# Optimization experiments

Measured on AMD Instinct MI355X. Metric: run time of the kernel, lower is better.

The kernel has to match this reference:

```python
import jax, jax.numpy as jnp
import numpy as np

B, S, D, H = 4, 2048, 768, 12


def setup_inputs() -> dict:
    key = jax.random.key(0)
    k1, k2, k3, k4 = jax.random.split(key, 4)
    std = D ** (-0.5)
    x = jax.random.normal(k1, (B, S, D), dtype=jnp.float32)
    W_QKV = jax.random.normal(k2, (3, D, D), dtype=jnp.float32) * std
    W_O = jax.random.normal(k3, (D, D), dtype=jnp.float32) * std
    token_positions = jnp.sort(jax.random.randint(k4, (B, S), 0, S), axis=-1).astype(jnp.int64)
    return {"x": x, "W_QKV": W_QKV, "W_O": W_O, "token_positions": token_positions,
            "num_heads": H, "theta": 10000}


def _apply_rope(t, cos, sin):
    # t: (B, H, S, Hd); cos/sin: (B, 1, S, Hd/2). Interleaved even/odd pairs.
    te, to = t[..., 0::2], t[..., 1::2]
    re = te * cos - to * sin
    ro = te * sin + to * cos
    return jnp.stack([re, ro], axis=-1).reshape(t.shape)


def reference(x, W_QKV, W_O, token_positions, num_heads, theta):
    b, s, d = x.shape
    hd = d // num_heads  # d_head = d_k = d_v
    # fused QKV projection: Q = x @ W_QKV[0].T etc.
    qkv = jnp.einsum('bsd,kod->kbso', x, W_QKV)              # (3, B, S, D)
    qkv = qkv.reshape(3, b, s, num_heads, hd).transpose(0, 1, 3, 2, 4)  # (3, B, H, S, Hd)
    q, k, v = qkv[0], qkv[1], qkv[2]
    # RoPE angles: pos * theta^(-2j/d_k)
    inv_freq = jnp.asarray(theta, x.dtype) ** (-(jnp.arange(0, hd, 2, dtype=x.dtype) / hd))
    angles = token_positions.astype(x.dtype)[..., None] * inv_freq    # (B, S, Hd/2)
    cos = jnp.cos(angles)[:, None]                                     # (B, 1, S, Hd/2)
    sin = jnp.sin(angles)[:, None]
    q = _apply_rope(q, cos, sin)
    k = _apply_rope(k, cos, sin)
    # causal attention
    scores = jnp.einsum('bhqd,bhkd->bhqk', q, k) / (hd ** 0.5)        # (B, H, S, S)
    causal = jnp.tril(jnp.ones((s, s), dtype=bool))
    scores = jnp.where(causal, scores, -jnp.inf)
    probs = jax.nn.softmax(scores, axis=-1)
    out = jnp.einsum('bhqk,bhkd->bhqd', probs, v)                      # (B, H, S, Hd)
    out = out.transpose(0, 2, 1, 3).reshape(b, s, d)
    return out @ W_O.T
```

## Files before the change

kernel.cpp:

```cpp
#include <hip/hip_runtime.h>
#include <hip/hip_bf16.h>

typedef __bf16 bf16;
typedef __bf16 bf16x8 __attribute__((ext_vector_type(8)));
typedef __bf16 bf16x4 __attribute__((ext_vector_type(4)));
typedef short  s16x4  __attribute__((ext_vector_type(4)));
typedef float  f32x4  __attribute__((ext_vector_type(4)));

#if defined(__has_builtin)
#if __has_builtin(__builtin_amdgcn_mfma_f32_16x16x16bf16_1k)
#define HAVE_MFMA16 1
#endif
#endif

__device__ __forceinline__ void gl_lds16(const void* g, void* l) {
  __builtin_amdgcn_global_load_lds(
      (__attribute__((address_space(1))) const void*)g,
      (__attribute__((address_space(3))) void*)l, 16, 0, 0);
}

__device__ __forceinline__ f32x4 mfma32(bf16x8 a, bf16x8 b, f32x4 c) {
  return __builtin_amdgcn_mfma_f32_16x16x32_bf16(a, b, c, 0, 0, 0);
}
#if HAVE_MFMA16
__device__ __forceinline__ f32x4 mfma16(s16x4 a, s16x4 b, f32x4 c) {
  return __builtin_amdgcn_mfma_f32_16x16x16bf16_1k(a, b, c, 0, 0, 0);
}
#endif

__global__ void cvtk(const float* __restrict__ src, bf16* __restrict__ dst, int n4) {
  int i = blockIdx.x * 256 + threadIdx.x;
  if (i < n4) {
    float4 v = ((const float4*)src)[i];
    bf16x4 o;
    o[0] = (bf16)v.x; o[1] = (bf16)v.y; o[2] = (bf16)v.z; o[3] = (bf16)v.w;
    ((bf16x4*)dst)[i] = o;
  }
}

template <int MODE>
__global__ void gemm_bt(const bf16* __restrict__ A, const bf16* __restrict__ Bm,
                        void* __restrict__ Cout) {
  constexpr int K = 768;
  __shared__ __align__(16) char As[128 * 64];
  __shared__ __align__(16) char Bs[128 * 64];
  const int tid = threadIdx.x;
  const int w = tid >> 6, lane = tid & 63;
  const int quad = lane >> 4, l15 = lane & 15;
  const int wrow = w >> 1, wcol = w & 1;
  const int m0 = blockIdx.x * 128, n0 = blockIdx.y * 128;

  f32x4 acc[4][4];
#pragma unroll
  for (int mt = 0; mt < 4; ++mt)
#pragma unroll
    for (int nt = 0; nt < 4; ++nt) acc[mt][nt] = (f32x4){0.f, 0.f, 0.f, 0.f};

  for (int k0 = 0; k0 < K; k0 += 32) {
    __syncthreads();
#pragma unroll
    for (int i = 0; i < 2; ++i) {
      int L = i * 256 + tid;
      int r = L >> 2, cl = L & 3;
      int cg = cl ^ ((r >> 1) & 3);
      gl_lds16(A + (size_t)(m0 + r) * K + k0 + cg * 8, As + (i * 256 + w * 64) * 16);
      gl_lds16(Bm + (size_t)(n0 + r) * K + k0 + cg * 8, Bs + (i * 256 + w * 64) * 16);
    }
    __syncthreads();

    bf16x8 af[4], bfr[4];
#pragma unroll
    for (int mt = 0; mt < 4; ++mt) {
      int r = wrow * 64 + mt * 16 + l15;
      int cl = quad ^ ((r >> 1) & 3);
      af[mt] = *(const bf16x8*)(As + r * 64 + cl * 16);
    }
#pragma unroll
    for (int nt = 0; nt < 4; ++nt) {
      int r = wcol * 64 + nt * 16 + l15;
      int cl = quad ^ ((r >> 1) & 3);
      bfr[nt] = *(const bf16x8*)(Bs + r * 64 + cl * 16);
    }
#pragma unroll
    for (int mt = 0; mt < 4; ++mt)
#pragma unroll
      for (int nt = 0; nt < 4; ++nt)
        acc[mt][nt] = mfma32(af[mt], bfr[nt], acc[mt][nt]);
  }

#pragma unroll
  for (int mt = 0; mt < 4; ++mt)
#pragma unroll
    for (int nt = 0; nt < 4; ++nt)
#pragma unroll
      for (int r = 0; r < 4; ++r) {
        int m = m0 + wrow * 64 + mt * 16 + quad * 4 + r;
        int n = n0 + wcol * 64 + nt * 16 + l15;
        float v = acc[mt][nt][r];
        if (MODE == 0) {
          ((float*)Cout)[(size_t)m * 768 + n] = v;
        } else {
          int mat = n / 768, rem = n % 768;
          int h = rem >> 6, d = rem & 63;
          int b = m >> 11, s = m & 2047;
          ((bf16*)Cout)[(((size_t)(mat * 4 + b) * 12 + h) * 2048 + s) * 64 + d] = (bf16)v;
        }
      }
}

__global__ void rope_k(bf16* __restrict__ qk, const int* __restrict__ tpos,
                       const int* __restrict__ thetap) {
  int i = blockIdx.x * 256 + threadIdx.x;
  int d2 = i & 31;
  int s = (i >> 5) & 2047;
  int rest = i >> 16;
  int rb = rest / 12;
  int b = rb & 3;
  size_t off = ((size_t)rest * 2048 + s) * 64 + d2 * 2;
  int pos = tpos[b * 2048 + s];
  float lt = log2f((float)(*thetap));
  float fr = exp2f(-(float)d2 * (1.0f / 32.0f) * lt);
  float ang = (float)pos * fr;
  float sn, cs;
  sincosf(ang, &sn, &cs);
  float te = (float)qk[off], to = (float)qk[off + 1];
  qk[off]     = (bf16)(te * cs - to * sn);
  qk[off + 1] = (bf16)(te * sn + to * cs);
}

__global__ void vtrans(const bf16* __restrict__ v, bf16* __restrict__ vt) {
  __shared__ bf16 t[64][80];
  int bh = blockIdx.x >> 5, st = blockIdx.x & 31;
  int tid = threadIdx.x;
  const bf16* vin = v + (size_t)bh * 2048 * 64 + (size_t)st * 64 * 64;
#pragma unroll
  for (int i = 0; i < 2; ++i) {
    int L = i * 256 + tid;
    int sl = L >> 3, d0 = (L & 7) * 8;
    bf16x8 x = *(const bf16x8*)(vin + sl * 64 + d0);
#pragma unroll
    for (int j = 0; j < 8; ++j) t[d0 + j][sl] = x[j];
  }
  __syncthreads();
  bf16* vo = vt + (size_t)bh * 64 * 2048 + st * 64;
#pragma unroll
  for (int i = 0; i < 2; ++i) {
    int L = i * 256 + tid;
    int dl = L >> 3, s0 = (L & 7) * 8;
    bf16x8 y;
#pragma unroll
    for (int j = 0; j < 8; ++j) y[j] = t[dl][s0 + j];
    *(bf16x8*)(vo + (size_t)dl * 2048 + s0) = y;
  }
}

__global__ void attn(const bf16* __restrict__ qkv, const bf16* __restrict__ vt,
                     bf16* __restrict__ aout) {
  const float SC = 0.125f * 1.44269504088896f;
  const int bx = blockIdx.x;
  const int qt = 31 - (bx / 48);
  const int bh = bx % 48;
  const int b = bh / 12, h = bh % 12;
  const int tid = threadIdx.x, w = tid >> 6, lane = tid & 63;
  const int quad = lane >> 4, l15 = lane & 15;
  const bf16* Q  = qkv + (size_t)bh * (2048 * 64);
  const bf16* Kp = qkv + (size_t)(48 + bh) * (2048 * 64);
  const bf16* Vt = vt + (size_t)bh * (64 * 2048);
  __shared__ __align__(16) char Ks[2][64 * 128];
  __shared__ __align__(16) char Vs[2][64 * 128];

  const int qi = qt * 64 + w * 16 + l15;
  bf16x8 qf0 = *(const bf16x8*)(Q + (size_t)qi * 64 + quad * 8);
  bf16x8 qf1 = *(const bf16x8*)(Q + (size_t)qi * 64 + 32 + quad * 8);

  float mi = -1e30f, li = 0.f;
  f32x4 o[4];
#pragma unroll
  for (int dt = 0; dt < 4; ++dt) o[dt] = (f32x4){0.f, 0.f, 0.f, 0.f};

  auto stage = [&](int kb, int bufi) {
#pragma unroll
    for (int i = 0; i < 2; ++i) {
      int L = i * 256 + tid;
      int r = L >> 3, cl = L & 7, cg = cl ^ (r & 7);
      gl_lds16(Kp + (size_t)(kb * 64 + r) * 64 + cg * 8, Ks[bufi] + (i * 256 + w * 64) * 16);
      gl_lds16(Vt + (size_t)r * 2048 + kb * 64 + cg * 8, Vs[bufi] + (i * 256 + w * 64) * 16);
    }
  };

  stage(0, 0);
  int buf = 0;

  for (int kb = 0; kb <= qt; ++kb) {
    __syncthreads();
    if (kb < qt) stage(kb + 1, buf ^ 1);
    const char* Kb = Ks[buf];
    const char* Vb = Vs[buf];

    float S[16];
#pragma unroll
    for (int sk = 0; sk < 4; ++sk) {
      int r = sk * 16 + l15;
      int cl0 = quad ^ (r & 7);
      int cl1 = (4 + quad) ^ (r & 7);
      bf16x8 kf0 = *(const bf16x8*)(Kb + r * 128 + cl0 * 16);
      bf16x8 kf1 = *(const bf16x8*)(Kb + r * 128 + cl1 * 16);
      f32x4 st = (f32x4){0.f, 0.f, 0.f, 0.f};
      st = mfma32(kf0, qf0, st);
      st = mfma32(kf1, qf1, st);
#pragma unroll
      for (int rr = 0; rr < 4; ++rr) S[sk * 4 + rr] = st[rr] * SC;
    }
    if (kb == qt) {
#pragma unroll
      for (int sk = 0; sk < 4; ++sk)
#pragma unroll
        for (int rr = 0; rr < 4; ++rr) {
          int key = kb * 64 + sk * 16 + quad * 4 + rr;
          if (key > qi) S[sk * 4 + rr] = -1e30f;
        }
    }

    float bm = S[0];
#pragma unroll
    for (int j = 1; j < 16; ++j) bm = fmaxf(bm, S[j]);
    bm = fmaxf(bm, __shfl_xor(bm, 16));
    bm = fmaxf(bm, __shfl_xor(bm, 32));
    float mn = fmaxf(mi, bm);
    float alpha = exp2f(mi - mn);
    float rs = 0.f;
#if HAVE_MFMA16
    s16x4 pf[4];
#endif
#pragma unroll
    for (int sk = 0; sk < 4; ++sk) {
      bf16x4 pb;
#pragma unroll
      for (int rr = 0; rr < 4; ++rr) {
        float p = exp2f(S[sk * 4 + rr] - mn);
        rs += p;
        S[sk * 4 + rr] = p;
        pb[rr] = (bf16)p;
      }
#if HAVE_MFMA16
      pf[sk] = __builtin_bit_cast(s16x4, pb);
#else
      (void)pb;
#endif
    }
    rs += __shfl_xor(rs, 16);
    rs += __shfl_xor(rs, 32);
    li = li * alpha + rs;
    mi = mn;

    float ar[4];
#pragma unroll
    for (int rr = 0; rr < 4; ++rr) ar[rr] = __shfl(alpha, quad * 4 + rr);
#pragma unroll
    for (int dt = 0; dt < 4; ++dt)
#pragma unroll
      for (int rr = 0; rr < 4; ++rr) o[dt][rr] *= ar[rr];

#if HAVE_MFMA16
#pragma unroll
    for (int sk = 0; sk < 4; ++sk)
#pragma unroll
      for (int dt = 0; dt < 4; ++dt) {
        int rr = dt * 16 + l15;
        int c = sk * 2 + (quad >> 1);
        int cl = c ^ (rr & 7);
        s16x4 vf = *(const s16x4*)(Vb + rr * 128 + cl * 16 + (quad & 1) * 8);
        o[dt] = mfma16(pf[sk], vf, o[dt]);
      }
#else
#pragma unroll
    for (int kc = 0; kc < 2; ++kc) {
      bf16x8 af;
#pragma unroll
      for (int j = 0; j < 8; ++j) {
        int sq = (quad & 1) * 2 + (j >> 2);
        int src = sq * 16 + l15;
        float v0 = __shfl(S[kc * 8 + (j & 3)], src);
        float v1 = __shfl(S[kc * 8 + 4 + (j & 3)], src);
        af[j] = (bf16)((quad < 2) ? v0 : v1);
      }
#pragma unroll
      for (int dt = 0; dt < 4; ++dt) {
        int rr = dt * 16 + l15;
        int c = kc * 4 + quad;
        int cl = c ^ (rr & 7);
        bf16x8 vf = *(const bf16x8*)(Vb + rr * 128 + cl * 16);
        o[dt] = mfma32(af, vf, o[dt]);
      }
    }
#endif
    buf ^= 1;
  }

  float lr[4];
#pragma unroll
  for (int rr = 0; rr < 4; ++rr) lr[rr] = __shfl(li, quad * 4 + rr);
#pragma unroll
  for (int dt = 0; dt < 4; ++dt)
#pragma unroll
    for (int rr = 0; rr < 4; ++rr) {
      int q = qt * 64 + w * 16 + quad * 4 + rr;
      int n = h * 64 + dt * 16 + l15;
      aout[((size_t)b * 2048 + q) * 768 + n] = (bf16)(o[dt][rr] / lr[rr]);
    }
}

extern "C" void kernel_launch(void* const* d_in, const int* in_sizes, int n_in,
                              void* d_out, int out_size, void* d_ws, size_t ws_size,
                              hipStream_t stream) {
  const float* x    = (const float*)d_in[0];
  const float* wqkv = (const float*)d_in[1];
  const float* wo   = (const float*)d_in[2];
  const int* tpos   = (const int*)d_in[3];
  const int* thetap = (const int*)d_in[5];

  char* ws = (char*)d_ws;
  bf16* xb    = (bf16*)(ws);
  bf16* wqkvb = (bf16*)(ws + 12582912);
  bf16* wob   = (bf16*)(ws + 16121856);
  bf16* qkv   = (bf16*)(ws + 17301504);
  bf16* vtb   = (bf16*)(ws + 55050240);
  bf16* vptr  = qkv + (size_t)2 * 4 * 12 * 2048 * 64;

  cvtk<<<6144, 256, 0, stream>>>(x, xb, 1572864);
  cvtk<<<1728, 256, 0, stream>>>(wqkv, wqkvb, 442368);
  cvtk<<<576, 256, 0, stream>>>(wo, wob, 147456);
  gemm_bt<1><<<dim3(64, 18), 256, 0, stream>>>(xb, wqkvb, (void*)qkv);
  rope_k<<<24576, 256, 0, stream>>>(qkv, tpos, thetap);
  vtrans<<<1536, 256, 0, stream>>>(vptr, vtb);
  attn<<<1536, 256, 0, stream>>>(qkv, vtb, xb);
  gemm_bt<0><<<dim3(64, 6), 256, 0, stream>>>(xb, wob, d_out);
}
```

Measured before the change: 250.4 us.

## Use 128-row query tiles in attention, fold scale into RoPE, merge convert kernels

The attention kernel now runs 512-thread blocks that each cover 128 query rows, so every staged K/V tile in LDS is shared by eight waves instead of four. This halves the number of blocks and the K/V traffic per query. On the last key tile the first four waves skip the math because that tile is fully masked for them. The softmax scale and log2e factor are folded into Q during the RoPE pass, which removes a multiply per score. The three fp32-to-bf16 conversion launches are merged into a single kernel. In exchange, causal load balance is coarser and larger blocks may reduce occupancy.

```diff
diff --git a/kernel.cpp b/kernel.cpp
--- a/kernel.cpp
+++ b/kernel.cpp
@@ -28,14 +28,18 @@
 }
 #endif
 
-__global__ void cvtk(const float* __restrict__ src, bf16* __restrict__ dst, int n4) {
-  int i = blockIdx.x * 256 + threadIdx.x;
-  if (i < n4) {
-    float4 v = ((const float4*)src)[i];
-    bf16x4 o;
-    o[0] = (bf16)v.x; o[1] = (bf16)v.y; o[2] = (bf16)v.z; o[3] = (bf16)v.w;
-    ((bf16x4*)dst)[i] = o;
-  }
+__global__ void cvt3(const float* __restrict__ a, bf16* __restrict__ da,
+                     const float* __restrict__ b, bf16* __restrict__ db,
+                     const float* __restrict__ c, bf16* __restrict__ dc) {
+  int bx = blockIdx.x;
+  const float* s; bf16* d; int i;
+  if (bx < 6144)      { s = a; d = da; i = bx * 256 + threadIdx.x; }
+  else if (bx < 7872) { s = b; d = db; i = (bx - 6144) * 256 + threadIdx.x; }
+  else                { s = c; d = dc; i = (bx - 7872) * 256 + threadIdx.x; }
+  float4 v = ((const float4*)s)[i];
+  bf16x4 o;
+  o[0] = (bf16)v.x; o[1] = (bf16)v.y; o[2] = (bf16)v.z; o[3] = (bf16)v.w;
+  ((bf16x4*)d)[i] = o;
 }
 
 template <int MODE>
@@ -123,9 +127,10 @@
   float ang = (float)pos * fr;
   float sn, cs;
   sincosf(ang, &sn, &cs);
+  float scq = (rest < 48) ? 0.18033688011112042f : 1.0f;
   float te = (float)qk[off], to = (float)qk[off + 1];
-  qk[off]     = (bf16)(te * cs - to * sn);
-  qk[off + 1] = (bf16)(te * sn + to * cs);
+  qk[off]     = (bf16)((te * cs - to * sn) * scq);
+  qk[off + 1] = (bf16)((te * sn + to * cs) * scq);
 }
 
 __global__ void vtrans(const bf16* __restrict__ v, bf16* __restrict__ vt) {
@@ -154,11 +159,11 @@
   }
 }
 
-__global__ void attn(const bf16* __restrict__ qkv, const bf16* __restrict__ vt,
-                     bf16* __restrict__ aout) {
-  const float SC = 0.125f * 1.44269504088896f;
+__global__ __launch_bounds__(512, 8)
+void attn(const bf16* __restrict__ qkv, const bf16* __restrict__ vt,
+          bf16* __restrict__ aout) {
   const int bx = blockIdx.x;
-  const int qt = 31 - (bx / 48);
+  const int qt = 15 - (bx / 48);
   const int bh = bx % 48;
   const int b = bh / 12, h = bh % 12;
   const int tid = threadIdx.x, w = tid >> 6, lane = tid & 63;
@@ -169,7 +174,7 @@
   __shared__ __align__(16) char Ks[2][64 * 128];
   __shared__ __align__(16) char Vs[2][64 * 128];
 
-  const int qi = qt * 64 + w * 16 + l15;
+  const int qi = qt * 128 + w * 16 + l15;
   bf16x8 qf0 = *(const bf16x8*)(Q + (size_t)qi * 64 + quad * 8);
   bf16x8 qf1 = *(const bf16x8*)(Q + (size_t)qi * 64 + 32 + quad * 8);
 
@@ -179,21 +184,19 @@
   for (int dt = 0; dt < 4; ++dt) o[dt] = (f32x4){0.f, 0.f, 0.f, 0.f};
 
   auto stage = [&](int kb, int bufi) {
-#pragma unroll
-    for (int i = 0; i < 2; ++i) {
-      int L = i * 256 + tid;
-      int r = L >> 3, cl = L & 7, cg = cl ^ (r & 7);
-      gl_lds16(Kp + (size_t)(kb * 64 + r) * 64 + cg * 8, Ks[bufi] + (i * 256 + w * 64) * 16);
-      gl_lds16(Vt + (size_t)r * 2048 + kb * 64 + cg * 8, Vs[bufi] + (i * 256 + w * 64) * 16);
-    }
+    int r = tid >> 3, cl = tid & 7, cg = cl ^ (r & 7);
+    gl_lds16(Kp + (size_t)(kb * 64 + r) * 64 + cg * 8, Ks[bufi] + tid * 16);
+    gl_lds16(Vt + (size_t)r * 2048 + kb * 64 + cg * 8, Vs[bufi] + tid * 16);
   };
 
+  const int nTiles = 2 * qt + 2;
   stage(0, 0);
   int buf = 0;
 
-  for (int kb = 0; kb <= qt; ++kb) {
+  for (int kb = 0; kb < nTiles; ++kb) {
     __syncthreads();
-    if (kb < qt) stage(kb + 1, buf ^ 1);
+    if (kb + 1 < nTiles) stage(kb + 1, buf ^ 1);
+    if (kb == nTiles - 1 && w < 4) { buf ^= 1; continue; }
     const char* Kb = Ks[buf];
     const char* Vb = Vs[buf];
 
@@ -209,9 +212,9 @@
       st = mfma32(kf0, qf0, st);
       st = mfma32(kf1, qf1, st);
 #pragma unroll
-      for (int rr = 0; rr < 4; ++rr) S[sk * 4 + rr] = st[rr] * SC;
-    }
-    if (kb == qt) {
+      for (int rr = 0; rr < 4; ++rr) S[sk * 4 + rr] = st[rr];
+    }
+    if (kb >= 2 * qt) {
 #pragma unroll
       for (int sk = 0; sk < 4; ++sk)
 #pragma unroll
@@ -304,7 +307,7 @@
   for (int dt = 0; dt < 4; ++dt)
 #pragma unroll
     for (int rr = 0; rr < 4; ++rr) {
-      int q = qt * 64 + w * 16 + quad * 4 + rr;
+      int q = qt * 128 + w * 16 + quad * 4 + rr;
       int n = h * 64 + dt * 16 + l15;
       aout[((size_t)b * 2048 + q) * 768 + n] = (bf16)(o[dt][rr] / lr[rr]);
     }
@@ -327,12 +330,10 @@
   bf16* vtb   = (bf16*)(ws + 55050240);
   bf16* vptr  = qkv + (size_t)2 * 4 * 12 * 2048 * 64;
 
-  cvtk<<<6144, 256, 0, stream>>>(x, xb, 1572864);
-  cvtk<<<1728, 256, 0, stream>>>(wqkv, wqkvb, 442368);
-  cvtk<<<576, 256, 0, stream>>>(wo, wob, 147456);
+  cvt3<<<8448, 256, 0, stream>>>(x, xb, wqkv, wqkvb, wo, wob);
   gemm_bt<1><<<dim3(64, 18), 256, 0, stream>>>(xb, wqkvb, (void*)qkv);
   rope_k<<<24576, 256, 0, stream>>>(qkv, tpos, thetap);
   vtrans<<<1536, 256, 0, stream>>>(vptr, vtb);
-  attn<<<1536, 256, 0, stream>>>(qkv, vtb, xb);
+  attn<<<768, 512, 0, stream>>>(qkv, vtb, xb);
   gemm_bt<0><<<dim3(64, 6), 256, 0, stream>>>(xb, wob, d_out);
 }
```

After: 252.2 us. No clear change (+0.7%).
